# Kernel tuning notes

Measured on AMD Instinct MI355X. Metric: run time of the kernel, lower is better.

The kernel has to match this reference:

```python
import jax, jax.numpy as jnp
import numpy as np

D = 1024      # embedding_dim
H = 16        # num_heads
DH = D // H   # head_dim
DFF = 4 * D
EPS = 1e-5


def setup_inputs() -> dict:
    key = jax.random.key(0)
    ks = jax.random.split(key, 10)
    B, T = 2, 2048
    s = 0.02
    return {
        "x": jax.random.normal(ks[0], (B, T, D), dtype=jnp.float32),
        "Wq": jax.random.normal(ks[1], (H, D, DH), dtype=jnp.float32) * s,
        "Wk": jax.random.normal(ks[2], (H, D, DH), dtype=jnp.float32) * s,
        "Wv": jax.random.normal(ks[3], (H, D, DH), dtype=jnp.float32) * s,
        "W1": jax.random.normal(ks[4], (D, DFF), dtype=jnp.float32) * s,
        "b1": jnp.zeros((DFF,), dtype=jnp.float32),
        "W2": jax.random.normal(ks[5], (DFF, D), dtype=jnp.float32) * s,
        "b2": jnp.zeros((D,), dtype=jnp.float32),
        "gamma1": jnp.ones((D,), dtype=jnp.float32),
        "beta1": jnp.zeros((D,), dtype=jnp.float32),
        "gamma2": jnp.ones((D,), dtype=jnp.float32),
        "beta2": jnp.zeros((D,), dtype=jnp.float32),
    }


def _layernorm(x, gamma, beta):
    # torch.var default is unbiased (ddof=1) -- faithful to LayerNorm1d
    mean = jnp.mean(x, axis=-1, keepdims=True)
    var = jnp.var(x, axis=-1, keepdims=True, ddof=1)
    return gamma * (x - mean) * jax.lax.rsqrt(var + EPS) + beta


def _block(x, Wq, Wk, Wv, W1, b1, W2, b2, gamma1, beta1, gamma2, beta2):
    B, T, _ = x.shape
    h = _layernorm(x, gamma1, beta1)
    # per-head projections stacked: [B,H,T,DH]
    Q = jnp.einsum('btd,hde->bhte', h, Wq)
    K = jnp.einsum('btd,hde->bhte', h, Wk)
    V = jnp.einsum('btd,hde->bhte', h, Wv)
    # NOTE: original scales by 1/sqrt(embedding_dim), NOT head_dim
    scores = jnp.einsum('bhqe,bhke->bhqk', Q, K) / jnp.sqrt(jnp.float32(D))
    causal = jnp.tril(jnp.ones((T, T), dtype=bool))
    scores = jnp.where(causal, scores, -jnp.inf)
    attn = jax.nn.softmax(scores, axis=-1)
    out = jnp.einsum('bhqk,bhke->bhqe', attn, V)
    # torch.cat over heads along last dim == transpose+reshape
    out = out.transpose(0, 2, 1, 3).reshape(B, T, D)
    x = x + out
    h2 = _layernorm(x, gamma2, beta2)
    ff = jax.nn.relu(h2 @ W1 + b1) @ W2 + b2  # dropout is identity at inference
    return x + ff


def reference(x, Wq, Wk, Wv, W1, b1, W2, b2, gamma1, beta1, gamma2, beta2):
    return _block(x, Wq, Wk, Wv, W1, b1, W2, b2, gamma1, beta1, gamma2, beta2)
```

## Files before the change

kernel.cpp:

```cpp
#include <hip/hip_runtime.h>

typedef unsigned short u16;
typedef __bf16 bf16;
typedef __attribute__((ext_vector_type(8))) __bf16 bf16x8;
typedef __attribute__((ext_vector_type(4))) float f32x4;
typedef __attribute__((ext_vector_type(8))) unsigned short u16x8;
typedef unsigned long long u64;

__device__ __forceinline__ float bf2f(u16 h) {
  return __uint_as_float(((unsigned int)h) << 16);
}
__device__ __forceinline__ u16 f2bf(float f) {
  unsigned int u = __float_as_uint(f);
  return (u16)((u + 0x7fffu + ((u >> 16) & 1u)) >> 16);
}
__device__ __forceinline__ u16 ld_cv(const void* p, size_t i, int f32) {
  return f32 ? f2bf(((const float*)p)[i]) : ((const u16*)p)[i];
}
__device__ __forceinline__ float ld_f(const void* p, size_t i, int f32) {
  return f32 ? ((const float*)p)[i] : bf2f(((const u16*)p)[i]);
}
__device__ __forceinline__ void async16(const u16* g, u16* l) {
  __builtin_amdgcn_global_load_lds(
      (const __attribute__((address_space(1))) unsigned int*)g,
      (__attribute__((address_space(3))) unsigned int*)l, 16, 0, 0);
}
__device__ __forceinline__ unsigned pk_bf16(float hi, float lo) {
  return __builtin_amdgcn_perm(__float_as_uint(hi) + 0x8000u,
                               __float_as_uint(lo) + 0x8000u, 0x07060302u);
}

__global__ void sniff_kernel(const u16* __restrict__ x, int* __restrict__ flag) {
  const int tid = threadIdx.x;
  int me = 0;
#pragma unroll
  for (int j = 0; j < 4; j++) {
    const u16 v = x[(tid * 4 + j) * 2];
    const int e = (v >> 7) & 0xFF;
    me = me > e ? me : e;
  }
#pragma unroll
  for (int off = 32; off > 0; off >>= 1) {
    const int o = __shfl_down(me, off);
    me = me > o ? me : o;
  }
  __shared__ int sm[4];
  if ((tid & 63) == 0) sm[tid >> 6] = me;
  __syncthreads();
  if (tid == 0) {
    int a = sm[0] > sm[1] ? sm[0] : sm[1];
    int b = sm[2] > sm[3] ? sm[2] : sm[3];
    *flag = ((a > b ? a : b) >= 140) ? 1 : 0;
  }
}

__global__ void prep_kernel(const void* __restrict__ Wq, const void* __restrict__ Wk,
                            const void* __restrict__ Wv, const void* __restrict__ W1,
                            const void* __restrict__ W2,
                            u16* __restrict__ WTq, u16* __restrict__ W1T,
                            u16* __restrict__ W2T, const int* __restrict__ flag) {
  __shared__ u16 tile[64][65];
  const int f = *flag;
  const int bid = blockIdx.x;
  const int lx = threadIdx.x & 63, ly = threadIdx.x >> 6;
  if (bid < 768) {
    const int bx = bid & 15, wh = bid >> 4;
    const int w = wh >> 4, hh = wh & 15;
    const int tr = bx * 64;
    const void* W = (w == 0) ? Wq : ((w == 1) ? Wk : Wv);
    const size_t hbase = (size_t)hh * 65536;
#pragma unroll
    for (int i = 0; i < 16; i++)
      tile[ly * 16 + i][lx] = ld_cv(W, hbase + (size_t)(tr + ly * 16 + i) * 64 + lx, f);
    __syncthreads();
#pragma unroll
    for (int i = 0; i < 16; i++)
      WTq[((size_t)(w * 1024 + hh * 64 + ly * 16 + i)) * 1024 + tr + lx] =
          tile[lx][ly * 16 + i];
  } else {
    const void* src;
    u16* dst;
    int R, C, tc, tr;
    if (bid < 1792) {
      const int j = bid - 768;
      src = W1; dst = W1T; R = 1024; C = 4096;
      tc = (j & 63) * 64; tr = (j >> 6) * 64;
    } else {
      const int j = bid - 1792;
      src = W2; dst = W2T; R = 4096; C = 1024;
      tc = (j & 15) * 64; tr = (j >> 4) * 64;
    }
#pragma unroll
    for (int i = 0; i < 16; i++)
      tile[ly * 16 + i][lx] = ld_cv(src, (size_t)(tr + ly * 16 + i) * C + tc + lx, f);
    __syncthreads();
#pragma unroll
    for (int i = 0; i < 16; i++)
      dst[(size_t)(tc + ly * 16 + i) * R + tr + lx] = tile[lx][ly * 16 + i];
  }
}

template <int EPI, int WR, int WC, bool MS>
__launch_bounds__(WR * WC * 64)
__global__ void gemm_bt(const u16* __restrict__ A, const u16* __restrict__ B,
                        int K, int NX, int N,
                        const void* __restrict__ bias, const u16* __restrict__ res,
                        void* __restrict__ out,
                        u16* __restrict__ Qo, u16* __restrict__ Ko, u16* __restrict__ Vto,
                        const int* __restrict__ flag) {
  constexpr int BM = WR * 64, BN = WC * 64, T = WR * WC * 64;
  constexpr int RPA = T / 4;
  constexpr int RAH = BM / RPA;
  constexpr int RBH = BN / RPA;
  __shared__ __align__(16) u16 As[BM * 64];
  __shared__ __align__(16) u16 Bs[BN * 64];
  const int tid = threadIdx.x;
  const int bid = blockIdx.x;
  const int sxp = NX >> 3;
  const int xcd = bid & 7, j9 = bid >> 3;
  int m0, n0;
  if (MS) {
    m0 = (xcd * sxp + j9 % sxp) * BM;
    n0 = (j9 / sxp) * BN;
  } else {
    n0 = (xcd * sxp + j9 % sxp) * BN;
    m0 = (j9 / sxp) * BM;
  }
  const int wave = tid >> 6, lane = tid & 63;
  const int wm = (wave / WC) * 64, wn = (wave % WC) * 64;
  const int lm = lane & 15, lq = lane >> 4;
  const int fb = (EPI >= 1) ? *flag : 0;

  const f32x4 zero = {0.f, 0.f, 0.f, 0.f};
  f32x4 acc[4][4];
#pragma unroll
  for (int i = 0; i < 4; i++)
#pragma unroll
    for (int j = 0; j < 4; j++) acc[i][j] = zero;

  const int ar = tid >> 2;
  const int ac = (tid & 3) * 8;
  const u16* Ag = A + (size_t)(m0 + ar) * K + ac;
  const u16* Bg = B + (size_t)(n0 + ar) * K + ac;
  u16* AsP = &As[tid * 8];
  u16* BsP = &Bs[tid * 8];

  for (int k0 = 0; k0 < K; k0 += 64) {
#pragma unroll
    for (int hh = 0; hh < 2; hh++) {
#pragma unroll
      for (int c = 0; c < RAH; c++)
        async16(Ag + k0 + hh * 32 + (size_t)c * RPA * K,
                AsP + hh * BM * 32 + c * RPA * 32);
#pragma unroll
      for (int c = 0; c < RBH; c++)
        async16(Bg + k0 + hh * 32 + (size_t)c * RPA * K,
                BsP + hh * BN * 32 + c * RPA * 32);
    }
    __syncthreads();
    bf16x8 a0[4], a1[4], b0[4], b1[4];
#pragma unroll
    for (int i = 0; i < 4; i++) {
      a0[i] = *(const bf16x8*)&As[(wm + i * 16 + lm) * 32 + lq * 8];
      a1[i] = *(const bf16x8*)&As[BM * 32 + (wm + i * 16 + lm) * 32 + lq * 8];
    }
#pragma unroll
    for (int i = 0; i < 4; i++) {
      b0[i] = *(const bf16x8*)&Bs[(wn + i * 16 + lm) * 32 + lq * 8];
      b1[i] = *(const bf16x8*)&Bs[BN * 32 + (wn + i * 16 + lm) * 32 + lq * 8];
    }
#pragma unroll
    for (int i = 0; i < 4; i++)
#pragma unroll
      for (int j = 0; j < 4; j++) {
        acc[i][j] = __builtin_amdgcn_mfma_f32_16x16x32_bf16(a0[i], b0[j], acc[i][j], 0, 0, 0);
        acc[i][j] = __builtin_amdgcn_mfma_f32_16x16x32_bf16(a1[i], b1[j], acc[i][j], 0, 0, 0);
      }
    __syncthreads();
  }

  if (EPI == 0) {
#pragma unroll
    for (int i = 0; i < 4; i++) {
      const int row0 = m0 + wm + i * 16 + lq * 4;
      const int bb = row0 >> 11, t0 = row0 & 2047;
#pragma unroll
      for (int j = 0; j < 4; j++) {
        const int col = n0 + wn + j * 16 + lm;
        const int w = col >> 10, nn = col & 1023;
        const int hh = nn >> 6, e = nn & 63;
        if (w == 2) {
          ushort4 v4;
          v4.x = f2bf(acc[i][j][0]);
          v4.y = f2bf(acc[i][j][1]);
          v4.z = f2bf(acc[i][j][2]);
          v4.w = f2bf(acc[i][j][3]);
          *(ushort4*)&Vto[(((size_t)(bb * 16 + hh)) * 64 + e) * 2048 + t0] = v4;
        } else {
          u16* dst = (w == 0) ? Qo : Ko;
#pragma unroll
          for (int r = 0; r < 4; r++)
            dst[(((size_t)(bb * 16 + hh)) * 2048 + t0 + r) * 64 + e] =
                f2bf(acc[i][j][r]);
        }
      }
    }
  } else {
#pragma unroll
    for (int i = 0; i < 4; i++) {
#pragma unroll
      for (int r = 0; r < 4; r++) {
        const int row = m0 + wm + i * 16 + lq * 4 + r;
#pragma unroll
        for (int j = 0; j < 4; j++) {
          const int col = n0 + wn + j * 16 + lm;
          const float c = acc[i][j][r];
          if (EPI == 1) {
            const float v = c + ld_f(bias, col, fb);
            ((u16*)out)[(size_t)row * N + col] = f2bf(v > 0.f ? v : 0.f);
          } else {
            const float v = c + ld_f(bias, col, fb) + bf2f(res[(size_t)row * N + col]);
            if (fb)
              ((float*)out)[(size_t)row * N + col] = v;
            else
              ((u16*)out)[(size_t)row * N + col] = f2bf(v);
          }
        }
      }
    }
  }
}

__launch_bounds__(256)
__global__ void gemm_sk(const u16* __restrict__ A, const u16* __restrict__ B,
                        const void* __restrict__ bias, const u16* __restrict__ res,
                        void* __restrict__ out, const int* __restrict__ flag) {
  __shared__ __align__(16) unsigned char smem[33536];
  u16* As = (u16*)smem;
  u16* Bs = (u16*)smem + 8192;
  float* Ml = (float*)smem;
  const int tid = threadIdx.x;
  const int bid = blockIdx.x;
  const int xcd = bid & 7, j9 = bid >> 3;
  const int m0 = (xcd * 4 + j9 % 4) * 128;
  const int n0 = (j9 / 4) * 64;
  const int wave = tid >> 6, lane = tid & 63;
  const int wm = (wave & 1) * 64, kh = wave >> 1;
  const int lm = lane & 15, lq = lane >> 4;
  const int fb = *flag;

  const f32x4 zero = {0.f, 0.f, 0.f, 0.f};
  f32x4 acc[4][4];
#pragma unroll
  for (int i = 0; i < 4; i++)
#pragma unroll
    for (int j = 0; j < 4; j++) acc[i][j] = zero;

  const int ar = tid >> 2;
  const int ac = (tid & 3) * 8;
  const u16* Ag = A + (size_t)(m0 + ar) * 4096 + ac;
  const u16* Bg = B + (size_t)(n0 + ar) * 4096 + ac;
  const int khash = kh * 4096;
  const int khbs = kh * 2048;

  for (int k0 = 0; k0 < 2048; k0 += 32) {
#pragma unroll
    for (int khh = 0; khh < 2; khh++) {
#pragma unroll
      for (int c = 0; c < 2; c++)
        async16(Ag + khh * 2048 + k0 + (size_t)c * 64 * 4096,
                As + khh * 4096 + c * 2048 + tid * 8);
      async16(Bg + khh * 2048 + k0, Bs + khh * 2048 + tid * 8);
    }
    __syncthreads();
    bf16x8 a[4], b[4];
#pragma unroll
    for (int i = 0; i < 4; i++)
      a[i] = *(const bf16x8*)&As[khash + (wm + i * 16 + lm) * 32 + lq * 8];
#pragma unroll
    for (int j = 0; j < 4; j++)
      b[j] = *(const bf16x8*)&Bs[khbs + (j * 16 + lm) * 32 + lq * 8];
#pragma unroll
    for (int i = 0; i < 4; i++)
#pragma unroll
      for (int j = 0; j < 4; j++)
        acc[i][j] = __builtin_amdgcn_mfma_f32_16x16x32_bf16(a[i], b[j], acc[i][j], 0, 0, 0);
    __syncthreads();
  }

  __syncthreads();
  if (kh == 1) {
    const int mh = wave & 1;
#pragma unroll
    for (int i = 0; i < 4; i++)
#pragma unroll
      for (int j = 0; j < 4; j++)
#pragma unroll
        for (int r = 0; r < 4; r++)
          Ml[mh * 4160 + (i * 16 + lq * 4 + r) * 65 + j * 16 + lm] = acc[i][j][r];
  }
  __syncthreads();
  if (kh == 0) {
    const int mh = wave & 1;
#pragma unroll
    for (int i = 0; i < 4; i++) {
#pragma unroll
      for (int r = 0; r < 4; r++) {
        const int row = m0 + wm + i * 16 + lq * 4 + r;
#pragma unroll
        for (int j = 0; j < 4; j++) {
          const int col = n0 + j * 16 + lm;
          const float c = acc[i][j][r] +
                          Ml[mh * 4160 + (i * 16 + lq * 4 + r) * 65 + j * 16 + lm];
          const float v = c + ld_f(bias, col, fb) + bf2f(res[(size_t)row * 1024 + col]);
          if (fb)
            ((float*)out)[(size_t)row * 1024 + col] = v;
          else
            ((u16*)out)[(size_t)row * 1024 + col] = f2bf(v);
        }
      }
    }
  }
}

__launch_bounds__(256)
__global__ void attn_mfma(const u16* __restrict__ Q, const u16* __restrict__ K,
                          const u16* __restrict__ Vt, const void* __restrict__ xres,
                          const int* __restrict__ flag, u16* __restrict__ x2) {
  __shared__ __align__(16) unsigned char smem[35328];
  const int tid = threadIdx.x;
  const int wave = tid >> 6, lane = tid & 63;
  const int lm = lane & 15, quad = lane >> 4;
  const int bid = blockIdx.x;
  const int xcd = bid & 7, jj = bid >> 3;
  const int bh = xcd + 8 * (jj & 3);
  const int pair = jj >> 2;
  const int b = bh >> 4, h = bh & 15;
  const int f32in = *flag;

  u16* stw = (u16*)smem + wave * 4096;
  u16* Ksw = stw;
  u16* Vsw = stw + 2048;
  float (*Olds)[32][68] = (float(*)[32][68])smem;
  float (*Llds)[2][16] = (float(*)[2][16])(smem + 34816);

  const u16* Kbh = K + (size_t)bh * 131072;
  const u16* Vbh = Vt + (size_t)bh * 131072;
  const f32x4 zero = {0.f, 0.f, 0.f, 0.f};
  const int srow = lane >> 2;
  const int schk = (lane & 3) * 8;

  union V8 { bf16x8 v; struct { u64 lo, hi; } q; };

#pragma unroll 1
  for (int phase = 0; phase < 2; phase++) {
    const int qb = phase ? (63 - pair) : pair;
    const int qw0 = qb * 32;

    bf16x8 qf[2][2];
#pragma unroll
    for (int s = 0; s < 2; s++) {
      const u16* Qp = Q + ((size_t)bh * 2048 + qw0 + s * 16 + lm) * 64 + quad * 8;
      qf[s][0] = *(const bf16x8*)Qp;
      qf[s][1] = *(const bf16x8*)(Qp + 32);
    }
    f32x4 ot[2][4];
#pragma unroll
    for (int s = 0; s < 2; s++)
#pragma unroll
      for (int j = 0; j < 4; j++) ot[s][j] = zero;
    float l[2] = {0.f, 0.f};

    const int nt = qb + 1;
    const int si = (nt * wave) >> 2;
    const int ei = (nt * (wave + 1)) >> 2;

    for (int t = si; t < ei; t++) {
      const int ks = t * 32;
#pragma unroll
      for (int hh2 = 0; hh2 < 2; hh2++)
#pragma unroll
        for (int c = 0; c < 2; c++)
          async16(Kbh + (size_t)(ks + c * 16 + srow) * 64 + hh2 * 32 + schk,
                  Ksw + hh2 * 1024 + c * 512 + lane * 8);
#pragma unroll
      for (int c = 0; c < 4; c++)
        async16(Vbh + (size_t)(c * 16 + srow) * 2048 + ks + schk,
                Vsw + c * 512 + lane * 8);
      __builtin_amdgcn_s_waitcnt(0x0F70);

      f32x4 S[2][2];
#pragma unroll
      for (int s = 0; s < 2; s++)
#pragma unroll
        for (int hh = 0; hh < 2; hh++) {
          const bf16x8 k0 = *(const bf16x8*)&Ksw[(hh * 16 + lm) * 32 + quad * 8];
          const bf16x8 k1 = *(const bf16x8*)&Ksw[1024 + (hh * 16 + lm) * 32 + quad * 8];
          f32x4 a = zero;
          a = __builtin_amdgcn_mfma_f32_16x16x32_bf16(k0, qf[s][0], a, 0, 0, 0);
          a = __builtin_amdgcn_mfma_f32_16x16x32_bf16(k1, qf[s][1], a, 0, 0, 0);
          S[s][hh] = a;
        }
      const bool maskT = (t == qb);
#pragma unroll
      for (int s = 0; s < 2; s++) {
        float p[2][4];
#pragma unroll
        for (int hh = 0; hh < 2; hh++)
#pragma unroll
          for (int r = 0; r < 4; r++) {
            float v = __expf(S[s][hh][r] * 0.03125f);
            if (maskT && (hh * 16 + quad * 4 + r > s * 16 + lm)) v = 0.f;
            l[s] += v;
            p[hh][r] = v;
          }
        unsigned pk[4];
        pk[0] = pk_bf16(p[0][1], p[0][0]);
        pk[1] = pk_bf16(p[0][3], p[0][2]);
        pk[2] = pk_bf16(p[1][1], p[1][0]);
        pk[3] = pk_bf16(p[1][3], p[1][2]);
        const bf16x8 pf = *(const bf16x8*)pk;
#pragma unroll
        for (int j = 0; j < 4; j++) {
          V8 vf;
          vf.q.lo = *(const u64*)&Vsw[(j * 16 + lm) * 32 + quad * 4];
          vf.q.hi = *(const u64*)&Vsw[(j * 16 + lm) * 32 + 16 + quad * 4];
          ot[s][j] = __builtin_amdgcn_mfma_f32_16x16x32_bf16(vf.v, pf, ot[s][j], 0, 0, 0);
        }
      }
    }

#pragma unroll
    for (int s = 0; s < 2; s++) {
      l[s] += __shfl_xor(l[s], 16);
      l[s] += __shfl_xor(l[s], 32);
    }

    __syncthreads();

#pragma unroll
    for (int s = 0; s < 2; s++)
#pragma unroll
      for (int j = 0; j < 4; j++)
        *(f32x4*)&Olds[wave][s * 16 + lm][j * 16 + quad * 4] = ot[s][j];
    if (quad == 0) {
      Llds[wave][0][lm] = l[0];
      Llds[wave][1][lm] = l[1];
    }
    __syncthreads();
    const int q = tid >> 3;
    const int e0 = (tid & 7) * 8;
    f32x4 oa = zero, ob = zero;
#pragma unroll
    for (int w = 0; w < 4; w++) {
      oa += *(const f32x4*)&Olds[w][q][e0];
      ob += *(const f32x4*)&Olds[w][q][e0 + 4];
    }
    const float lt = Llds[0][q >> 4][q & 15] + Llds[1][q >> 4][q & 15] +
                     Llds[2][q >> 4][q & 15] + Llds[3][q >> 4][q & 15];
    const float linv = 1.f / lt;
    const size_t rowbase = ((size_t)(b * 2048 + qw0 + q)) * 1024 + h * 64 + e0;
    float xv[8];
    if (f32in) {
      const float* xf = (const float*)xres + rowbase;
      const float4 u0 = *(const float4*)xf;
      const float4 u1 = *(const float4*)(xf + 4);
      xv[0] = u0.x; xv[1] = u0.y; xv[2] = u0.z; xv[3] = u0.w;
      xv[4] = u1.x; xv[5] = u1.y; xv[6] = u1.z; xv[7] = u1.w;
    } else {
      const u16x8 u = *(const u16x8*)((const u16*)xres + rowbase);
#pragma unroll
      for (int k = 0; k < 8; k++) xv[k] = bf2f(u[k]);
    }
    u16x8 o8;
#pragma unroll
    for (int k = 0; k < 4; k++) o8[k] = f2bf(xv[k] + oa[k] * linv);
#pragma unroll
    for (int k = 0; k < 4; k++) o8[4 + k] = f2bf(xv[4 + k] + ob[k] * linv);
    *(u16x8*)&x2[rowbase] = o8;
    __syncthreads();
  }
}

__launch_bounds__(256)
__global__ void ln_kernel(const void* __restrict__ x, const void* __restrict__ gamma,
                          const void* __restrict__ beta, u16* __restrict__ out,
                          const int* __restrict__ flag, int xraw) {
  const size_t row = blockIdx.x;
  const int tid = threadIdx.x;
  const int f = *flag;
  const int fx = xraw ? f : 0;
  float v0, v1, v2, v3;
  if (fx) {
    const float4 v = *((const float4*)x + row * 256 + tid);
    v0 = v.x; v1 = v.y; v2 = v.z; v3 = v.w;
  } else {
    const ushort4 u = *((const ushort4*)x + row * 256 + tid);
    v0 = bf2f(u.x); v1 = bf2f(u.y); v2 = bf2f(u.z); v3 = bf2f(u.w);
  }
  float s = v0 + v1 + v2 + v3;
  float sq = v0 * v0 + v1 * v1 + v2 * v2 + v3 * v3;
#pragma unroll
  for (int off = 32; off > 0; off >>= 1) {
    s += __shfl_down(s, off);
    sq += __shfl_down(sq, off);
  }
  __shared__ float ss[4], ssq[4];
  if ((tid & 63) == 0) { ss[tid >> 6] = s; ssq[tid >> 6] = sq; }
  __syncthreads();
  s = ss[0] + ss[1] + ss[2] + ss[3];
  sq = ssq[0] + ssq[1] + ssq[2] + ssq[3];
  const float mean = s * (1.f / 1024.f);
  const float var = (sq - 1024.f * mean * mean) * (1.f / 1023.f);
  const float rs = rsqrtf(var + 1e-5f);
  const int c0 = tid * 4;
  ushort4 o;
  o.x = f2bf(ld_f(gamma, c0 + 0, f) * (v0 - mean) * rs + ld_f(beta, c0 + 0, f));
  o.y = f2bf(ld_f(gamma, c0 + 1, f) * (v1 - mean) * rs + ld_f(beta, c0 + 1, f));
  o.z = f2bf(ld_f(gamma, c0 + 2, f) * (v2 - mean) * rs + ld_f(beta, c0 + 2, f));
  o.w = f2bf(ld_f(gamma, c0 + 3, f) * (v3 - mean) * rs + ld_f(beta, c0 + 3, f));
  *(ushort4*)&out[row * 1024 + tid * 4] = o;
}

extern "C" void kernel_launch(void* const* d_in, const int* in_sizes, int n_in,
                              void* d_out, int out_size, void* d_ws, size_t ws_size,
                              hipStream_t stream) {
  const void* x      = d_in[0];
  const void* Wq     = d_in[1];
  const void* Wk     = d_in[2];
  const void* Wv     = d_in[3];
  const void* W1     = d_in[4];
  const void* b1     = d_in[5];
  const void* W2     = d_in[6];
  const void* b2     = d_in[7];
  const void* gamma1 = d_in[8];
  const void* beta1  = d_in[9];
  const void* gamma2 = d_in[10];
  const void* beta2  = d_in[11];
  u16* ws = (u16*)d_ws;

  const size_t M4 = 4194304;
  u16* h   = ws;
  u16* Qb  = ws + 1 * M4;
  u16* Kb  = ws + 2 * M4;
  u16* Vtb = ws + 3 * M4;
  u16* WTq = ws + 4 * M4;
  u16* x2  = ws + 4 * M4;
  u16* h2  = ws + 5 * M4;
  u16* W1T = ws + 6 * M4;
  u16* W2T = ws + 7 * M4;
  u16* ff1 = ws;
  int* flag = (int*)(ws + 8 * M4 + 9216);

  sniff_kernel<<<1, 256, 0, stream>>>((const u16*)x, flag);
  prep_kernel<<<2816, 256, 0, stream>>>(Wq, Wk, Wv, W1, W2, WTq, W1T, W2T, flag);
  ln_kernel<<<4096, 256, 0, stream>>>(x, gamma1, beta1, h, flag, 1);
  gemm_bt<0, 4, 2, false><<<384, 512, 0, stream>>>(h, WTq, 1024, 24, 3072,
                                                   nullptr, nullptr, nullptr,
                                                   Qb, Kb, Vtb, flag);
  attn_mfma<<<1024, 256, 0, stream>>>(Qb, Kb, Vtb, x, flag, x2);
  ln_kernel<<<4096, 256, 0, stream>>>(x2, gamma2, beta2, h2, flag, 0);
  gemm_bt<1, 4, 2, false><<<512, 512, 0, stream>>>(h2, W1T, 1024, 32, 4096,
                                                   b1, nullptr, ff1,
                                                   nullptr, nullptr, nullptr, flag);
  gemm_sk<<<512, 256, 0, stream>>>(ff1, W2T, b2, x2, d_out, flag);
}
```

Before: 349.2 us.

## Triple-buffer split-K GEMM loads with async prefetch and LDS swizzle

Turns the gemm_sk main loop into a three-stage ring buffer in shared memory. Tiles two steps ahead are prefetched with async global-to-LDS loads, and explicit vmcnt waits replace the full syncthreads. It also XOR-swizzles the 16-byte column chunks to cut LDS bank conflicts on the fragment reads. The goal is to hide global load latency behind MFMA work, at the cost of more shared memory (72KB), which may lower occupancy.

```diff
diff --git a/kernel.cpp b/kernel.cpp
--- a/kernel.cpp
+++ b/kernel.cpp
@@ -235,9 +235,7 @@
 __global__ void gemm_sk(const u16* __restrict__ A, const u16* __restrict__ B,
                         const void* __restrict__ bias, const u16* __restrict__ res,
                         void* __restrict__ out, const int* __restrict__ flag) {
-  __shared__ __align__(16) unsigned char smem[33536];
-  u16* As = (u16*)smem;
-  u16* Bs = (u16*)smem + 8192;
+  __shared__ __align__(16) unsigned char smem[73728];
   float* Ml = (float*)smem;
   const int tid = threadIdx.x;
   const int bid = blockIdx.x;
@@ -257,36 +255,61 @@
     for (int j = 0; j < 4; j++) acc[i][j] = zero;
 
   const int ar = tid >> 2;
-  const int ac = (tid & 3) * 8;
-  const u16* Ag = A + (size_t)(m0 + ar) * 4096 + ac;
-  const u16* Bg = B + (size_t)(n0 + ar) * 4096 + ac;
-  const int khash = kh * 4096;
-  const int khbs = kh * 2048;
-
-  for (int k0 = 0; k0 < 2048; k0 += 32) {
+  const int sw = ((tid & 3) ^ ((tid >> 3) & 3)) * 8;
+  const u16* Ag = A + (size_t)(m0 + ar) * 4096 + sw;
+  const u16* Bg = B + (size_t)(n0 + ar) * 4096 + sw;
+  const int rsw = (lq ^ ((lm >> 1) & 3)) * 8;
+
+  auto stage = [&](int t, int off) {
+    const int k0 = t * 32;
+    u16* As_ = (u16*)smem + off;
 #pragma unroll
     for (int khh = 0; khh < 2; khh++) {
-#pragma unroll
-      for (int c = 0; c < 2; c++)
-        async16(Ag + khh * 2048 + k0 + (size_t)c * 64 * 4096,
-                As + khh * 4096 + c * 2048 + tid * 8);
-      async16(Bg + khh * 2048 + k0, Bs + khh * 2048 + tid * 8);
-    }
-    __syncthreads();
+      async16(Ag + khh * 2048 + k0, As_ + khh * 4096 + tid * 8);
+      async16(Ag + khh * 2048 + k0 + (size_t)64 * 4096,
+              As_ + khh * 4096 + 2048 + tid * 8);
+      async16(Bg + khh * 2048 + k0, As_ + 8192 + khh * 2048 + tid * 8);
+    }
+  };
+  auto compute = [&](int off) {
+    const u16* S = (const u16*)smem + off;
     bf16x8 a[4], b[4];
 #pragma unroll
     for (int i = 0; i < 4; i++)
-      a[i] = *(const bf16x8*)&As[khash + (wm + i * 16 + lm) * 32 + lq * 8];
+      a[i] = *(const bf16x8*)&S[kh * 4096 + (wm + i * 16 + lm) * 32 + rsw];
 #pragma unroll
     for (int j = 0; j < 4; j++)
-      b[j] = *(const bf16x8*)&Bs[khbs + (j * 16 + lm) * 32 + lq * 8];
+      b[j] = *(const bf16x8*)&S[8192 + kh * 2048 + (j * 16 + lm) * 32 + rsw];
 #pragma unroll
     for (int i = 0; i < 4; i++)
 #pragma unroll
       for (int j = 0; j < 4; j++)
         acc[i][j] = __builtin_amdgcn_mfma_f32_16x16x32_bf16(a[i], b[j], acc[i][j], 0, 0, 0);
-    __syncthreads();
-  }
+  };
+
+  stage(0, 0);
+  stage(1, 12288);
+  int cur = 0;
+  for (int t = 0; t < 62; t++) {
+    int c2 = cur + 2;
+    if (c2 >= 3) c2 -= 3;
+    stage(t + 2, c2 * 12288);
+    asm volatile("s_waitcnt vmcnt(12)" ::: "memory");
+    __builtin_amdgcn_s_barrier();
+    compute(cur * 12288);
+    __builtin_amdgcn_s_barrier();
+    cur = cur + 1;
+    if (cur == 3) cur = 0;
+  }
+  asm volatile("s_waitcnt vmcnt(6)" ::: "memory");
+  __builtin_amdgcn_s_barrier();
+  compute(cur * 12288);
+  __builtin_amdgcn_s_barrier();
+  cur = cur + 1;
+  if (cur == 3) cur = 0;
+  asm volatile("s_waitcnt vmcnt(0)" ::: "memory");
+  __builtin_amdgcn_s_barrier();
+  compute(cur * 12288);
 
   __syncthreads();
   if (kh == 1) {
```

After: 346.5 us. No clear change (-0.7%).

## Replace intra-block split-K FFN2 GEMM with grid split-K plus reduce kernel

Applied to the files above, without the earlier changes.

The second FFN GEMM used to split K across waves inside one block and reduce the halves through LDS. It now runs the generic 256x128 gemm_bt tile with a grid-level split-K of 2 that writes fp32 partials to workspace. A separate elementwise kernel then sums the partials and adds bias and residual. This reuses the larger, more efficient tile, at the cost of an extra kernel launch and about 32 MB of extra fp32 partial traffic.

```diff
diff --git a/kernel.cpp b/kernel.cpp
--- a/kernel.cpp
+++ b/kernel.cpp
@@ -103,7 +103,7 @@
 template <int EPI, int WR, int WC, bool MS>
 __launch_bounds__(WR * WC * 64)
 __global__ void gemm_bt(const u16* __restrict__ A, const u16* __restrict__ B,
-                        int K, int NX, int N,
+                        int K, int KLD, int NX, int N,
                         const void* __restrict__ bias, const u16* __restrict__ res,
                         void* __restrict__ out,
                         u16* __restrict__ Qo, u16* __restrict__ Ko, u16* __restrict__ Vto,
@@ -118,8 +118,13 @@
   const int bid = blockIdx.x;
   const int sxp = NX >> 3;
   const int xcd = bid & 7, j9 = bid >> 3;
-  int m0, n0;
-  if (MS) {
+  int m0, n0, koff = 0, khb = 0;
+  if (EPI == 3) {
+    m0 = (xcd * 2 + (j9 & 1)) * BM;
+    n0 = ((j9 >> 1) & 7) * BN;
+    khb = (j9 >> 4) & 1;
+    koff = khb * K;
+  } else if (MS) {
     m0 = (xcd * sxp + j9 % sxp) * BM;
     n0 = (j9 / sxp) * BN;
   } else {
@@ -129,7 +134,7 @@
   const int wave = tid >> 6, lane = tid & 63;
   const int wm = (wave / WC) * 64, wn = (wave % WC) * 64;
   const int lm = lane & 15, lq = lane >> 4;
-  const int fb = (EPI >= 1) ? *flag : 0;
+  const int fb = (EPI == 1 || EPI == 2) ? *flag : 0;
 
   const f32x4 zero = {0.f, 0.f, 0.f, 0.f};
   f32x4 acc[4][4];
@@ -140,8 +145,8 @@
 
   const int ar = tid >> 2;
   const int ac = (tid & 3) * 8;
-  const u16* Ag = A + (size_t)(m0 + ar) * K + ac;
-  const u16* Bg = B + (size_t)(n0 + ar) * K + ac;
+  const u16* Ag = A + (size_t)(m0 + ar) * KLD + koff + ac;
+  const u16* Bg = B + (size_t)(n0 + ar) * KLD + koff + ac;
   u16* AsP = &As[tid * 8];
   u16* BsP = &Bs[tid * 8];
 
@@ -150,11 +155,11 @@
     for (int hh = 0; hh < 2; hh++) {
 #pragma unroll
       for (int c = 0; c < RAH; c++)
-        async16(Ag + k0 + hh * 32 + (size_t)c * RPA * K,
+        async16(Ag + k0 + hh * 32 + (size_t)c * RPA * KLD,
                 AsP + hh * BM * 32 + c * RPA * 32);
 #pragma unroll
       for (int c = 0; c < RBH; c++)
-        async16(Bg + k0 + hh * 32 + (size_t)c * RPA * K,
+        async16(Bg + k0 + hh * 32 + (size_t)c * RPA * KLD,
                 BsP + hh * BN * 32 + c * RPA * 32);
     }
     __syncthreads();
@@ -202,6 +207,20 @@
           for (int r = 0; r < 4; r++)
             dst[(((size_t)(bb * 16 + hh)) * 2048 + t0 + r) * 64 + e] =
                 f2bf(acc[i][j][r]);
+        }
+      }
+    }
+  } else if (EPI == 3) {
+    float* P = khb ? (float*)Ko : (float*)Qo;
+#pragma unroll
+    for (int i = 0; i < 4; i++) {
+#pragma unroll
+      for (int r = 0; r < 4; r++) {
+        const int row = m0 + wm + i * 16 + lq * 4 + r;
+#pragma unroll
+        for (int j = 0; j < 4; j++) {
+          const int col = n0 + wn + j * 16 + lm;
+          P[(size_t)row * N + col] = acc[i][j][r];
         }
       }
     }
@@ -232,94 +251,31 @@
 }
 
 __launch_bounds__(256)
-__global__ void gemm_sk(const u16* __restrict__ A, const u16* __restrict__ B,
-                        const void* __restrict__ bias, const u16* __restrict__ res,
-                        void* __restrict__ out, const int* __restrict__ flag) {
-  __shared__ __align__(16) unsigned char smem[33536];
-  u16* As = (u16*)smem;
-  u16* Bs = (u16*)smem + 8192;
-  float* Ml = (float*)smem;
-  const int tid = threadIdx.x;
-  const int bid = blockIdx.x;
-  const int xcd = bid & 7, j9 = bid >> 3;
-  const int m0 = (xcd * 4 + j9 % 4) * 128;
-  const int n0 = (j9 / 4) * 64;
-  const int wave = tid >> 6, lane = tid & 63;
-  const int wm = (wave & 1) * 64, kh = wave >> 1;
-  const int lm = lane & 15, lq = lane >> 4;
-  const int fb = *flag;
-
-  const f32x4 zero = {0.f, 0.f, 0.f, 0.f};
-  f32x4 acc[4][4];
-#pragma unroll
-  for (int i = 0; i < 4; i++)
-#pragma unroll
-    for (int j = 0; j < 4; j++) acc[i][j] = zero;
-
-  const int ar = tid >> 2;
-  const int ac = (tid & 3) * 8;
-  const u16* Ag = A + (size_t)(m0 + ar) * 4096 + ac;
-  const u16* Bg = B + (size_t)(n0 + ar) * 4096 + ac;
-  const int khash = kh * 4096;
-  const int khbs = kh * 2048;
-
-  for (int k0 = 0; k0 < 2048; k0 += 32) {
-#pragma unroll
-    for (int khh = 0; khh < 2; khh++) {
-#pragma unroll
-      for (int c = 0; c < 2; c++)
-        async16(Ag + khh * 2048 + k0 + (size_t)c * 64 * 4096,
-                As + khh * 4096 + c * 2048 + tid * 8);
-      async16(Bg + khh * 2048 + k0, Bs + khh * 2048 + tid * 8);
-    }
-    __syncthreads();
-    bf16x8 a[4], b[4];
-#pragma unroll
-    for (int i = 0; i < 4; i++)
-      a[i] = *(const bf16x8*)&As[khash + (wm + i * 16 + lm) * 32 + lq * 8];
-#pragma unroll
-    for (int j = 0; j < 4; j++)
-      b[j] = *(const bf16x8*)&Bs[khbs + (j * 16 + lm) * 32 + lq * 8];
-#pragma unroll
-    for (int i = 0; i < 4; i++)
-#pragma unroll
-      for (int j = 0; j < 4; j++)
-        acc[i][j] = __builtin_amdgcn_mfma_f32_16x16x32_bf16(a[i], b[j], acc[i][j], 0, 0, 0);
-    __syncthreads();
-  }
-
-  __syncthreads();
-  if (kh == 1) {
-    const int mh = wave & 1;
-#pragma unroll
-    for (int i = 0; i < 4; i++)
-#pragma unroll
-      for (int j = 0; j < 4; j++)
-#pragma unroll
-        for (int r = 0; r < 4; r++)
-          Ml[mh * 4160 + (i * 16 + lq * 4 + r) * 65 + j * 16 + lm] = acc[i][j][r];
-  }
-  __syncthreads();
-  if (kh == 0) {
-    const int mh = wave & 1;
-#pragma unroll
-    for (int i = 0; i < 4; i++) {
-#pragma unroll
-      for (int r = 0; r < 4; r++) {
-        const int row = m0 + wm + i * 16 + lq * 4 + r;
-#pragma unroll
-        for (int j = 0; j < 4; j++) {
-          const int col = n0 + j * 16 + lm;
-          const float c = acc[i][j][r] +
-                          Ml[mh * 4160 + (i * 16 + lq * 4 + r) * 65 + j * 16 + lm];
-          const float v = c + ld_f(bias, col, fb) + bf2f(res[(size_t)row * 1024 + col]);
-          if (fb)
-            ((float*)out)[(size_t)row * 1024 + col] = v;
-          else
-            ((u16*)out)[(size_t)row * 1024 + col] = f2bf(v);
-        }
-      }
-    }
+__global__ void ffn2_reduce(const float* __restrict__ P0, const float* __restrict__ P1,
+                            const void* __restrict__ bias, const u16* __restrict__ res,
+                            void* __restrict__ out, const int* __restrict__ flag) {
+  const int f = *flag;
+  const size_t i0 = ((size_t)blockIdx.x * 256 + threadIdx.x) * 8;
+  const int col = (int)(i0 & 1023);
+  const float4 a0 = *(const float4*)(P0 + i0);
+  const float4 a1 = *(const float4*)(P0 + i0 + 4);
+  const float4 b0 = *(const float4*)(P1 + i0);
+  const float4 b1 = *(const float4*)(P1 + i0 + 4);
+  const u16x8 r8 = *(const u16x8*)(res + i0);
+  float v[8] = {a0.x + b0.x, a0.y + b0.y, a0.z + b0.z, a0.w + b0.w,
+                a1.x + b1.x, a1.y + b1.y, a1.z + b1.z, a1.w + b1.w};
+#pragma unroll
+  for (int k = 0; k < 8; k++) v[k] += ld_f(bias, col + k, f) + bf2f(r8[k]);
+  if (f) {
+    float4 o0 = {v[0], v[1], v[2], v[3]};
+    float4 o1 = {v[4], v[5], v[6], v[7]};
+    *(float4*)((float*)out + i0) = o0;
+    *(float4*)((float*)out + i0 + 4) = o1;
+  } else {
+    u16x8 o8;
+#pragma unroll
+    for (int k = 0; k < 8; k++) o8[k] = f2bf(v[k]);
+    *(u16x8*)((u16*)out + i0) = o8;
   }
 }
 
@@ -550,18 +506,23 @@
   u16* W1T = ws + 6 * M4;
   u16* W2T = ws + 7 * M4;
   u16* ff1 = ws;
+  float* P0 = (float*)(ws + 1 * M4);
+  float* P1 = (float*)(ws + 5 * M4);
   int* flag = (int*)(ws + 8 * M4 + 9216);
 
   sniff_kernel<<<1, 256, 0, stream>>>((const u16*)x, flag);
   prep_kernel<<<2816, 256, 0, stream>>>(Wq, Wk, Wv, W1, W2, WTq, W1T, W2T, flag);
   ln_kernel<<<4096, 256, 0, stream>>>(x, gamma1, beta1, h, flag, 1);
-  gemm_bt<0, 4, 2, false><<<384, 512, 0, stream>>>(h, WTq, 1024, 24, 3072,
+  gemm_bt<0, 4, 2, false><<<384, 512, 0, stream>>>(h, WTq, 1024, 1024, 24, 3072,
                                                    nullptr, nullptr, nullptr,
                                                    Qb, Kb, Vtb, flag);
   attn_mfma<<<1024, 256, 0, stream>>>(Qb, Kb, Vtb, x, flag, x2);
   ln_kernel<<<4096, 256, 0, stream>>>(x2, gamma2, beta2, h2, flag, 0);
-  gemm_bt<1, 4, 2, false><<<512, 512, 0, stream>>>(h2, W1T, 1024, 32, 4096,
+  gemm_bt<1, 4, 2, false><<<512, 512, 0, stream>>>(h2, W1T, 1024, 1024, 32, 4096,
                                                    b1, nullptr, ff1,
                                                    nullptr, nullptr, nullptr, flag);
-  gemm_sk<<<512, 256, 0, stream>>>(ff1, W2T, b2, x2, d_out, flag);
-}
+  gemm_bt<3, 4, 2, false><<<256, 512, 0, stream>>>(ff1, W2T, 2048, 4096, 8, 1024,
+                                                   nullptr, nullptr, nullptr,
+                                                   (u16*)P0, (u16*)P1, nullptr, flag);
+  ffn2_reduce<<<2048, 256, 0, stream>>>(P0, P1, b2, x2, d_out, flag);
+}
```

Result: no change. 346.1 us (-0.9%).
